# Kernel optimization log

Measured on AMD Instinct MI355X. Metric: run time of the kernel, lower is better.

## Reference

```python
import jax, jax.numpy as jnp
import numpy as np


def sym_logm(x):
    # matrix log of symmetric positive-definite matrices via eigh
    w, v = jnp.linalg.eigh(x)
    return jnp.einsum('...ik,...k,...jk->...ij', v, jnp.log(w), v)


def olm_diffeo(x):
    s = sym_logm(x)
    L = jnp.tril(s, -1)
    return L + L.swapaxes(-1, -2)


def cayley_map(X):
    I = jnp.eye(X.shape[-1], dtype=X.dtype)
    return (I - X) @ jnp.linalg.inv(I + X)


def trans_base(W, y):
    # C = cayley(skew(W)); y -> sym off-diagonal part of C y C^T
    C = cayley_map(W - W.T)
    y = jnp.einsum('pq,bnqr,sr->bnps', C, y, C)
    L = jnp.tril(y, -1)
    return L + L.swapaxes(-1, -2)


def setup_inputs() -> dict:
    B, N, n = 16, 512, 32
    key = jax.random.key(0)
    k1, k2, k3, k4 = jax.random.split(key, 4)
    A = jax.random.normal(k1, (B, N, n, n), dtype=jnp.float32)
    cov = A @ A.swapaxes(-1, -2) / n + jnp.eye(n, dtype=jnp.float32)
    d = jnp.sqrt(jnp.diagonal(cov, axis1=-2, axis2=-1))
    x = cov / (d[..., :, None] * d[..., None, :])  # SPD correlation matrices
    q_weight = jax.random.normal(k2, (n, n), dtype=jnp.float32) * 2.0 - 1.0
    k_weight = jax.random.normal(k3, (n, n), dtype=jnp.float32) * 2.0 - 1.0
    v_weight = jax.random.normal(k4, (n, n), dtype=jnp.float32) * 2.0 - 1.0
    return {"x": x, "q_weight": q_weight, "k_weight": k_weight, "v_weight": v_weight}


def reference(x, q_weight, k_weight, v_weight):
    xl = olm_diffeo(x)                       # [B,N,n,n]
    q = trans_base(q_weight, xl)
    k = trans_base(k_weight, xl)
    v = trans_base(v_weight, xl)
    B, N, n, _ = q.shape
    qf = q.reshape(B, N, n * n)
    kf = k.reshape(B, N, n * n)
    # energy[b,j,i] = ||q_i - k_j||_F  (Gram trick instead of [B,N,N,n,n] broadcast)
    q2 = jnp.sum(qf * qf, axis=-1)
    k2 = jnp.sum(kf * kf, axis=-1)
    d2 = q2[:, None, :] + k2[:, :, None] - 2.0 * jnp.einsum('bjf,bif->bji', kf, qf)
    energy = jnp.sqrt(jnp.maximum(d2, 1e-12))
    scores = 1.0 / (1.0 + jnp.log1p(energy))
    p = jax.nn.softmax(scores, axis=-2)      # softmax over j (dim -2), as in torch
    attn = p.swapaxes(-1, -2)                # [b, i, j]
    # out[b,c] = sum_a v[b,a] * attn[b,a,c]  (faithful to torch broadcast+sum(dim=1))
    return jnp.einsum('bac,baij->bcij', attn, v)
```

## Files before the change

### kernel.cpp

```cpp
#include <hip/hip_runtime.h>
#include <math.h>

#define NB 16
#define NSQ 512
#define NMAT (NB*NSQ)
#define NF 1024
#define NSWEEP 7
#define SB 36

__global__ __launch_bounds__(64) void cayley_kernel(
    const float* __restrict__ qw, const float* __restrict__ kw,
    const float* __restrict__ vw, float* __restrict__ Cout) {
  __shared__ float M[32][33];
  __shared__ float R[32][33];
  __shared__ float fac[32];
  const float* W = (blockIdx.x == 0) ? qw : ((blockIdx.x == 1) ? kw : vw);
  const int t = threadIdx.x;
  for (int idx = t; idx < 1024; idx += 64) {
    int i = idx >> 5, j = idx & 31;
    float xv = W[i*32+j] - W[j*32+i];
    float d = (i == j) ? 1.0f : 0.0f;
    M[i][j] = d - xv;
    R[i][j] = d + xv;
  }
  __syncthreads();
  for (int k = 0; k < 32; ++k) {
    float inv = 1.0f / M[k][k];
    __syncthreads();
    if (t < 32) M[k][t] *= inv; else R[k][t-32] *= inv;
    __syncthreads();
    if (t < 32) fac[t] = M[t][k];
    __syncthreads();
    if (t < 32) {
      float mk = M[k][t];
      for (int i = 0; i < 32; ++i) {
        if (i == k) continue;
        M[i][t] -= fac[i] * mk;
      }
    } else {
      int tc = t - 32;
      float rk = R[k][tc];
      for (int i = 0; i < 32; ++i) {
        if (i == k) continue;
        R[i][tc] -= fac[i] * rk;
      }
    }
    __syncthreads();
  }
  for (int idx = t; idx < 1024; idx += 64) {
    int p = idx >> 5, q = idx & 31;
    Cout[blockIdx.x * 1024 + idx] = R[q][p];
  }
}

__global__ __launch_bounds__(64) void logm_qkv_kernel(
    const float* __restrict__ x, const float* __restrict__ Cm,
    float* __restrict__ qo, float* __restrict__ ko, float* __restrict__ vo,
    float* __restrict__ q2, float* __restrict__ k2) {
  __shared__ __align__(16) float buf0[32*SB];
  __shared__ __align__(16) float buf1[32*SB];
  __shared__ __align__(16) float buf2[32*SB];
  __shared__ __align__(16) float2 cs[16];
  __shared__ __align__(16) float lw[32];
  const int t = threadIdx.x;
  const int m = blockIdx.x;
  const float* xm = x + (size_t)m * NF;

  #pragma unroll
  for (int s = 0; s < 4; ++s) {
    int fi = t + 64*s;
    int i = fi >> 3, j4 = (fi & 7) << 2;
    float4 xv = *(const float4*)&xm[(size_t)fi*4];
    *(float4*)&buf0[i*SB + j4] = xv;
    float4 iv;
    iv.x = (i == j4+0) ? 1.0f : 0.0f;
    iv.y = (i == j4+1) ? 1.0f : 0.0f;
    iv.z = (i == j4+2) ? 1.0f : 0.0f;
    iv.w = (i == j4+3) ? 1.0f : 0.0f;
    *(float4*)&buf1[i*SB + j4] = iv;
  }
  __syncthreads();

  const int ab = t >> 4;
  const int bI = t & 15;
  const int pi = ab & 1;

  for (int sw = 0; sw < NSWEEP; ++sw) {
    for (int r = 1; r < 32; ++r) {
      const int h = 31 - __builtin_clz((unsigned)r);
      const int lowmask = (1 << h) - 1;
      if (t < 16) {
        int p = ((t >> h) << (h+1)) | (t & lowmask);
        int q = p ^ r;
        float apq = buf0[p*SB+q];
        float c = 1.0f, s = 0.0f;
        if (fabsf(apq) > 1e-36f) {
          float app = buf0[p*SB+p];
          float aqq = buf0[q*SB+q];
          float tau = (aqq - app) / (2.0f * apq);
          float tt = 1.0f / (fabsf(tau) + sqrtf(1.0f + tau*tau));
          tt = (tau < 0.0f) ? -tt : tt;
          c = 1.0f / sqrtf(1.0f + tt*tt);
          s = tt * c;
        }
        cs[t] = make_float2(c, s);
      }
      __syncthreads();
      if (r == 1) {
        #pragma unroll
        for (int vtk = 0; vtk < 2; ++vtk) {
          int tsk = t + 64*vtk;
          int pr = tsk >> 3;
          int ch = (tsk & 7) << 2;
          int p = pr << 1;
          int q = p | 1;
          float2 c2 = cs[pr];
          float4 ap = *(float4*)&buf0[p*SB + ch];
          float4 aq = *(float4*)&buf0[q*SB + ch];
          float4 np, nq;
          np.x = c2.x*ap.x - c2.y*aq.x;  nq.x = fmaf(c2.y, ap.x, c2.x*aq.x);
          np.y = c2.x*ap.y - c2.y*aq.y;  nq.y = fmaf(c2.y, ap.y, c2.x*aq.y);
          np.z = c2.x*ap.z - c2.y*aq.z;  nq.z = fmaf(c2.y, ap.z, c2.x*aq.z);
          np.w = c2.x*ap.w - c2.y*aq.w;  nq.w = fmaf(c2.y, ap.w, c2.x*aq.w);
          *(float4*)&buf0[p*SB + ch] = np;
          *(float4*)&buf0[q*SB + ch] = nq;
        }
        __syncthreads();
        #pragma unroll
        for (int s4 = 0; s4 < 4; ++s4) {
          int tsk = t + 64*s4;
          int i = tsk >> 3;
          int cch = tsk & 7;
          float2 cA = cs[2*cch];
          float2 cB = cs[2*cch+1];
          float4 y = *(float4*)&buf0[i*SB + 4*cch];
          float4 z;
          z.x = cA.x*y.x - cA.y*y.y;  z.y = fmaf(cA.y, y.x, cA.x*y.y);
          z.z = cB.x*y.z - cB.y*y.w;  z.w = fmaf(cB.y, y.z, cB.x*y.w);
          *(float4*)&buf0[i*SB + 4*cch] = z;
        }
      } else {
        int pb = ((bI >> h) << (h+1)) | (bI & lowmask);
        int qb = pb ^ r;
        if (pi) { int tmp = pb; pb = qb; qb = tmp; }
        const float2 cb2 = cs[bI];
        const float cbb = cb2.x;
        const float sbb = pi ? -cb2.y : cb2.y;
        #pragma unroll
        for (int u = 0; u < 4; ++u) {
          int a = ab + 4*u;
          int pa = ((a >> h) << (h+1)) | (a & lowmask);
          int qa = pa ^ r;
          if (pi) { int tmp = pa; pa = qa; qa = tmp; }
          float2 ca2 = cs[a];
          float caa = ca2.x;
          float saa = pi ? -ca2.y : ca2.y;
          float* rp = buf0 + pa*SB;
          float* rq = buf0 + qa*SB;
          float x11 = rp[pb], x12 = rp[qb];
          float x21 = rq[pb], x22 = rq[qb];
          float y11 = caa*x11 - saa*x21;
          float y12 = caa*x12 - saa*x22;
          float y21 = fmaf(saa, x11, caa*x21);
          float y22 = fmaf(saa, x12, caa*x22);
          rp[pb] = cbb*y11 - sbb*y12;
          rp[qb] = fmaf(sbb, y11, cbb*y12);
          rq[pb] = cbb*y21 - sbb*y22;
          rq[qb] = fmaf(sbb, y21, cbb*y22);
        }
      }
      #pragma unroll
      for (int vtk = 0; vtk < 2; ++vtk) {
        int tsk = t + 64*vtk;
        int pr = tsk >> 3;
        int ch = (tsk & 7) << 2;
        int p = ((pr >> h) << (h+1)) | (pr & lowmask);
        int q = p ^ r;
        float2 c2 = cs[pr];
        float4 vp = *(float4*)&buf1[p*SB + ch];
        float4 vq = *(float4*)&buf1[q*SB + ch];
        float4 np, nq;
        np.x = c2.x*vp.x - c2.y*vq.x;  nq.x = fmaf(c2.y, vp.x, c2.x*vq.x);
        np.y = c2.x*vp.y - c2.y*vq.y;  nq.y = fmaf(c2.y, vp.y, c2.x*vq.y);
        np.z = c2.x*vp.z - c2.y*vq.z;  nq.z = fmaf(c2.y, vp.z, c2.x*vq.z);
        np.w = c2.x*vp.w - c2.y*vq.w;  nq.w = fmaf(c2.y, vp.w, c2.x*vq.w);
        *(float4*)&buf1[p*SB + ch] = np;
        *(float4*)&buf1[q*SB + ch] = nq;
      }
      __syncthreads();
    }
  }

  if (t < 32) lw[t] = logf(fmaxf(buf0[t*SB+t], 1e-30f));
  __syncthreads();
  #pragma unroll
  for (int s = 0; s < 16; ++s) {
    int idx = t + 64*s;
    int i = idx >> 5, k = idx & 31;
    buf0[i*SB + k] = buf1[k*SB + i];
  }
  __syncthreads();

  const int rg = t >> 3, cg = t & 7;
  const int i0 = rg*4, j0 = cg*4;
  {
    float acc[4][4] = {};
    #pragma unroll
    for (int k4 = 0; k4 < 32; k4 += 4) {
      float4 lv = *(float4*)&lw[k4];
      float4 av[4], bv[4];
      #pragma unroll
      for (int d = 0; d < 4; ++d) {
        float4 a4 = *(float4*)&buf0[(i0+d)*SB + k4];
        av[d].x = a4.x*lv.x; av[d].y = a4.y*lv.y; av[d].z = a4.z*lv.z; av[d].w = a4.w*lv.w;
        bv[d] = *(float4*)&buf0[(j0+d)*SB + k4];
      }
      #pragma unroll
      for (int d = 0; d < 4; ++d)
        #pragma unroll
        for (int e = 0; e < 4; ++e) {
          acc[d][e] = fmaf(av[d].x, bv[e].x, acc[d][e]);
          acc[d][e] = fmaf(av[d].y, bv[e].y, acc[d][e]);
          acc[d][e] = fmaf(av[d].z, bv[e].z, acc[d][e]);
          acc[d][e] = fmaf(av[d].w, bv[e].w, acc[d][e]);
        }
    }
    #pragma unroll
    for (int d = 0; d < 4; ++d) {
      if (rg == cg) acc[d][d] = 0.0f;
      float4 z; z.x = acc[d][0]; z.y = acc[d][1]; z.z = acc[d][2]; z.w = acc[d][3];
      *(float4*)&buf1[(i0+d)*SB + j0] = z;
    }
  }
  __syncthreads();

  for (int w = 0; w < 3; ++w) {
    const float* Cw = Cm + w*1024;
    #pragma unroll
    for (int s = 0; s < 4; ++s) {
      int fi = t + 64*s;
      int i = fi >> 3, c4 = (fi & 7) << 2;
      *(float4*)&buf0[i*SB + c4] = *(const float4*)&Cw[fi*4];
    }
    __syncthreads();
    {
      float acc[4][4] = {};
      #pragma unroll
      for (int k4 = 0; k4 < 32; k4 += 4) {
        float4 av[4], bv[4];
        #pragma unroll
        for (int d = 0; d < 4; ++d) {
          av[d] = *(float4*)&buf0[(i0+d)*SB + k4];
          bv[d] = *(float4*)&buf1[(j0+d)*SB + k4];
        }
        #pragma unroll
        for (int d = 0; d < 4; ++d)
          #pragma unroll
          for (int e = 0; e < 4; ++e) {
            acc[d][e] = fmaf(av[d].x, bv[e].x, acc[d][e]);
            acc[d][e] = fmaf(av[d].y, bv[e].y, acc[d][e]);
            acc[d][e] = fmaf(av[d].z, bv[e].z, acc[d][e]);
            acc[d][e] = fmaf(av[d].w, bv[e].w, acc[d][e]);
          }
      }
      #pragma unroll
      for (int d = 0; d < 4; ++d) {
        float4 z; z.x = acc[d][0]; z.y = acc[d][1]; z.z = acc[d][2]; z.w = acc[d][3];
        *(float4*)&buf2[(i0+d)*SB + j0] = z;
      }
    }
    __syncthreads();
    {
      float acc[4][4] = {};
      #pragma unroll
      for (int k4 = 0; k4 < 32; k4 += 4) {
        float4 av[4], bv[4];
        #pragma unroll
        for (int d = 0; d < 4; ++d) {
          av[d] = *(float4*)&buf2[(i0+d)*SB + k4];
          bv[d] = *(float4*)&buf0[(j0+d)*SB + k4];
        }
        #pragma unroll
        for (int d = 0; d < 4; ++d)
          #pragma unroll
          for (int e = 0; e < 4; ++e) {
            acc[d][e] = fmaf(av[d].x, bv[e].x, acc[d][e]);
            acc[d][e] = fmaf(av[d].y, bv[e].y, acc[d][e]);
            acc[d][e] = fmaf(av[d].z, bv[e].z, acc[d][e]);
            acc[d][e] = fmaf(av[d].w, bv[e].w, acc[d][e]);
          }
      }
      float ss = 0.0f;
      float* outp = (w == 0) ? qo : ((w == 1) ? ko : vo);
      #pragma unroll
      for (int d = 0; d < 4; ++d) {
        if (rg == cg) acc[d][d] = 0.0f;
        ss = fmaf(acc[d][0], acc[d][0], ss);
        ss = fmaf(acc[d][1], acc[d][1], ss);
        ss = fmaf(acc[d][2], acc[d][2], ss);
        ss = fmaf(acc[d][3], acc[d][3], ss);
        float4 z; z.x = acc[d][0]; z.y = acc[d][1]; z.z = acc[d][2]; z.w = acc[d][3];
        *(float4*)&outp[(size_t)m*NF + (i0+d)*32 + j0] = z;
      }
      if (w < 2) {
        #pragma unroll
        for (int off = 32; off > 0; off >>= 1)
          ss += __shfl_down(ss, off);
        if (t == 0) ((w == 0) ? q2 : k2)[m] = ss;
      }
    }
    __syncthreads();
  }
}

__global__ __launch_bounds__(256) void scores_kernel(
    const float* __restrict__ qf, const float* __restrict__ kf,
    const float* __restrict__ q2, const float* __restrict__ k2,
    float* __restrict__ P) {
  __shared__ float Ks[64][17];
  __shared__ float Qs[64][17];
  const int b = blockIdx.z;
  const int j0 = blockIdx.y * 64;
  const int i0 = blockIdx.x * 64;
  const int tx = threadIdx.x & 15, ty = threadIdx.x >> 4;
  const int lrow = threadIdx.x >> 2;
  const int lc4 = (threadIdx.x & 3) * 4;
  float acc[4][4] = {};
  const float* kb = kf + (size_t)(b*NSQ + j0) * NF;
  const float* qb = qf + (size_t)(b*NSQ + i0) * NF;
  for (int f0 = 0; f0 < NF; f0 += 16) {
    float4 kv = *(const float4*)(kb + (size_t)lrow*NF + f0 + lc4);
    float4 qv = *(const float4*)(qb + (size_t)lrow*NF + f0 + lc4);
    Ks[lrow][lc4+0] = kv.x; Ks[lrow][lc4+1] = kv.y; Ks[lrow][lc4+2] = kv.z; Ks[lrow][lc4+3] = kv.w;
    Qs[lrow][lc4+0] = qv.x; Qs[lrow][lc4+1] = qv.y; Qs[lrow][lc4+2] = qv.z; Qs[lrow][lc4+3] = qv.w;
    __syncthreads();
    #pragma unroll
    for (int kk = 0; kk < 16; ++kk) {
      float a0 = Ks[ty*4+0][kk], a1 = Ks[ty*4+1][kk], a2 = Ks[ty*4+2][kk], a3 = Ks[ty*4+3][kk];
      float b0 = Qs[tx*4+0][kk], b1 = Qs[tx*4+1][kk], b2 = Qs[tx*4+2][kk], b3 = Qs[tx*4+3][kk];
      acc[0][0]=fmaf(a0,b0,acc[0][0]); acc[0][1]=fmaf(a0,b1,acc[0][1]);
      acc[0][2]=fmaf(a0,b2,acc[0][2]); acc[0][3]=fmaf(a0,b3,acc[0][3]);
      acc[1][0]=fmaf(a1,b0,acc[1][0]); acc[1][1]=fmaf(a1,b1,acc[1][1]);
      acc[1][2]=fmaf(a1,b2,acc[1][2]); acc[1][3]=fmaf(a1,b3,acc[1][3]);
      acc[2][0]=fmaf(a2,b0,acc[2][0]); acc[2][1]=fmaf(a2,b1,acc[2][1]);
      acc[2][2]=fmaf(a2,b2,acc[2][2]); acc[2][3]=fmaf(a2,b3,acc[2][3]);
      acc[3][0]=fmaf(a3,b0,acc[3][0]); acc[3][1]=fmaf(a3,b1,acc[3][1]);
      acc[3][2]=fmaf(a3,b2,acc[3][2]); acc[3][3]=fmaf(a3,b3,acc[3][3]);
    }
    __syncthreads();
  }
  #pragma unroll
  for (int u = 0; u < 4; ++u) {
    int j = j0 + ty*4 + u;
    float kj = k2[b*NSQ + j];
    #pragma unroll
    for (int vv = 0; vv < 4; ++vv) {
      int i = i0 + tx*4 + vv;
      float d2 = kj + q2[b*NSQ + i] - 2.0f * acc[u][vv];
      float e = sqrtf(fmaxf(d2, 1e-12f));
      float sc = 1.0f / (1.0f + log1pf(e));
      P[(size_t)(b*NSQ + j)*NSQ + i] = sc;
    }
  }
}

__global__ __launch_bounds__(256) void softmax_kernel(float* __restrict__ P) {
  __shared__ float red[4][64];
  const int b = blockIdx.x >> 3;
  const int i0 = (blockIdx.x & 7) * 64;
  const int il = threadIdx.x & 63;
  const int jg = threadIdx.x >> 6;
  float* base = P + (size_t)b*NSQ*NSQ + i0 + il;
  float mx = -1e30f;
  for (int j = jg*128; j < jg*128 + 128; ++j)
    mx = fmaxf(mx, base[(size_t)j*NSQ]);
  red[jg][il] = mx;
  __syncthreads();
  float cm = fmaxf(fmaxf(red[0][il], red[1][il]), fmaxf(red[2][il], red[3][il]));
  float ssum = 0.0f;
  for (int j = jg*128; j < jg*128 + 128; ++j)
    ssum += expf(base[(size_t)j*NSQ] - cm);
  __syncthreads();
  red[jg][il] = ssum;
  __syncthreads();
  float inv = 1.0f / (red[0][il] + red[1][il] + red[2][il] + red[3][il]);
  for (int j = jg*128; j < jg*128 + 128; ++j) {
    size_t o = (size_t)j*NSQ;
    base[o] = expf(base[o] - cm) * inv;
  }
}

__global__ __launch_bounds__(256) void out_gemm_kernel(
    const float* __restrict__ P, const float* __restrict__ vf,
    float* __restrict__ out) {
  __shared__ float Ps[64][17];
  __shared__ float Vs[16][68];
  const int b = blockIdx.z;
  const int c0 = blockIdx.y * 64;
  const int f0 = blockIdx.x * 64;
  const int tx = threadIdx.x & 15, ty = threadIdx.x >> 4;
  float acc[4][4] = {};
  const float* Pb = P + (size_t)b * NSQ * NSQ;
  const float* Vb = vf + (size_t)b * NSQ * NF;
  for (int a0 = 0; a0 < NSQ; a0 += 16) {
    {
      int row = threadIdx.x >> 2;
      int c4 = (threadIdx.x & 3) * 4;
      float4 pv = *(const float4*)(Pb + (size_t)(c0 + row) * NSQ + a0 + c4);
      Ps[row][c4+0]=pv.x; Ps[row][c4+1]=pv.y; Ps[row][c4+2]=pv.z; Ps[row][c4+3]=pv.w;
    }
    {
      int row = threadIdx.x >> 4;
      int c4 = (threadIdx.x & 15) * 4;
      float4 vv4 = *(const float4*)(Vb + (size_t)(a0 + row) * NF + f0 + c4);
      Vs[row][c4+0]=vv4.x; Vs[row][c4+1]=vv4.y; Vs[row][c4+2]=vv4.z; Vs[row][c4+3]=vv4.w;
    }
    __syncthreads();
    #pragma unroll
    for (int kk = 0; kk < 16; ++kk) {
      float a0r = Ps[ty*4+0][kk], a1r = Ps[ty*4+1][kk], a2r = Ps[ty*4+2][kk], a3r = Ps[ty*4+3][kk];
      float b0 = Vs[kk][tx*4+0], b1 = Vs[kk][tx*4+1], b2 = Vs[kk][tx*4+2], b3 = Vs[kk][tx*4+3];
      acc[0][0]=fmaf(a0r,b0,acc[0][0]); acc[0][1]=fmaf(a0r,b1,acc[0][1]);
      acc[0][2]=fmaf(a0r,b2,acc[0][2]); acc[0][3]=fmaf(a0r,b3,acc[0][3]);
      acc[1][0]=fmaf(a1r,b0,acc[1][0]); acc[1][1]=fmaf(a1r,b1,acc[1][1]);
      acc[1][2]=fmaf(a1r,b2,acc[1][2]); acc[1][3]=fmaf(a1r,b3,acc[1][3]);
      acc[2][0]=fmaf(a2r,b0,acc[2][0]); acc[2][1]=fmaf(a2r,b1,acc[2][1]);
      acc[2][2]=fmaf(a2r,b2,acc[2][2]); acc[2][3]=fmaf(a2r,b3,acc[2][3]);
      acc[3][0]=fmaf(a3r,b0,acc[3][0]); acc[3][1]=fmaf(a3r,b1,acc[3][1]);
      acc[3][2]=fmaf(a3r,b2,acc[3][2]); acc[3][3]=fmaf(a3r,b3,acc[3][3]);
    }
    __syncthreads();
  }
  #pragma unroll
  for (int u = 0; u < 4; ++u) {
    float4 o;
    o.x = acc[u][0]; o.y = acc[u][1]; o.z = acc[u][2]; o.w = acc[u][3];
    *(float4*)(out + (size_t)(b*NSQ + c0 + ty*4 + u) * NF + f0 + tx*4) = o;
  }
}

extern "C" void kernel_launch(void* const* d_in, const int* in_sizes, int n_in,
                              void* d_out, int out_size, void* d_ws, size_t ws_size,
                              hipStream_t stream) {
  const float* x  = (const float*)d_in[0];
  const float* qw = (const float*)d_in[1];
  const float* kw = (const float*)d_in[2];
  const float* vw = (const float*)d_in[3];
  float* ws = (float*)d_ws;
  float* C  = ws;
  float* q  = ws + 3072;
  float* k  = q + (size_t)NMAT * NF;
  float* v  = k + (size_t)NMAT * NF;
  float* q2 = v + (size_t)NMAT * NF;
  float* k2 = q2 + NMAT;
  float* P  = k2 + NMAT;
  float* out = (float*)d_out;

  cayley_kernel<<<dim3(3), dim3(64), 0, stream>>>(qw, kw, vw, C);
  logm_qkv_kernel<<<dim3(NMAT), dim3(64), 0, stream>>>(x, C, q, k, v, q2, k2);
  scores_kernel<<<dim3(8, 8, NB), dim3(256), 0, stream>>>(q, k, q2, k2, P);
  softmax_kernel<<<dim3(NB * 8), dim3(256), 0, stream>>>(P);
  out_gemm_kernel<<<dim3(16, 8, NB), dim3(256), 0, stream>>>(P, v, out);
}
```

Before: 1.533 ms.

## Fold log-eigen reconstruction into per-weight transform using diagonal correction

Rather than forming the symmetric log matrix S = V diag(log w) V^T, zeroing its diagonal, and then computing C S C^T, the kernel computes D = C V directly and evaluates D diag(log w) D^T minus a correction term C diag(sd) C^T, where sd is the diagonal of S. This removes the explicit transpose and the separate 32x32x32 reconstruction GEMM and frees one shared buffer. Launch bounds now request 4 blocks per CU. In exchange, each of the three weight passes does an extra correction matmul. Subtracting large terms may also change rounding slightly.

New measurement: 2.517 ms. 1.64x slower.

```diff
diff --git a/kernel.cpp b/kernel.cpp
--- a/kernel.cpp
+++ b/kernel.cpp
@@ -53,15 +53,15 @@
   }
 }
 
-__global__ __launch_bounds__(64) void logm_qkv_kernel(
+__global__ __launch_bounds__(64, 4) void logm_qkv_kernel(
     const float* __restrict__ x, const float* __restrict__ Cm,
     float* __restrict__ qo, float* __restrict__ ko, float* __restrict__ vo,
     float* __restrict__ q2, float* __restrict__ k2) {
   __shared__ __align__(16) float buf0[32*SB];
   __shared__ __align__(16) float buf1[32*SB];
-  __shared__ __align__(16) float buf2[32*SB];
   __shared__ __align__(16) float2 cs[16];
   __shared__ __align__(16) float lw[32];
+  __shared__ __align__(16) float sd[32];
   const int t = threadIdx.x;
   const int m = blockIdx.x;
   const float* xm = x + (size_t)m * NF;
@@ -193,47 +193,18 @@
 
   if (t < 32) lw[t] = logf(fmaxf(buf0[t*SB+t], 1e-30f));
   __syncthreads();
-  #pragma unroll
-  for (int s = 0; s < 16; ++s) {
-    int idx = t + 64*s;
-    int i = idx >> 5, k = idx & 31;
-    buf0[i*SB + k] = buf1[k*SB + i];
+  if (t < 32) {
+    float s = 0.0f;
+    for (int k = 0; k < 32; ++k) {
+      float vv = buf1[k*SB + t];
+      s = fmaf(vv*vv, lw[k], s);
+    }
+    sd[t] = s;
   }
   __syncthreads();
 
   const int rg = t >> 3, cg = t & 7;
   const int i0 = rg*4, j0 = cg*4;
-  {
-    float acc[4][4] = {};
-    #pragma unroll
-    for (int k4 = 0; k4 < 32; k4 += 4) {
-      float4 lv = *(float4*)&lw[k4];
-      float4 av[4], bv[4];
-      #pragma unroll
-      for (int d = 0; d < 4; ++d) {
-        float4 a4 = *(float4*)&buf0[(i0+d)*SB + k4];
-        av[d].x = a4.x*lv.x; av[d].y = a4.y*lv.y; av[d].z = a4.z*lv.z; av[d].w = a4.w*lv.w;
-        bv[d] = *(float4*)&buf0[(j0+d)*SB + k4];
-      }
-      #pragma unroll
-      for (int d = 0; d < 4; ++d)
-        #pragma unroll
-        for (int e = 0; e < 4; ++e) {
-          acc[d][e] = fmaf(av[d].x, bv[e].x, acc[d][e]);
-          acc[d][e] = fmaf(av[d].y, bv[e].y, acc[d][e]);
-          acc[d][e] = fmaf(av[d].z, bv[e].z, acc[d][e]);
-          acc[d][e] = fmaf(av[d].w, bv[e].w, acc[d][e]);
-        }
-    }
-    #pragma unroll
-    for (int d = 0; d < 4; ++d) {
-      if (rg == cg) acc[d][d] = 0.0f;
-      float4 z; z.x = acc[d][0]; z.y = acc[d][1]; z.z = acc[d][2]; z.w = acc[d][3];
-      *(float4*)&buf1[(i0+d)*SB + j0] = z;
-    }
-  }
-  __syncthreads();
-
   for (int w = 0; w < 3; ++w) {
     const float* Cw = Cm + w*1024;
     #pragma unroll
@@ -243,57 +214,62 @@
       *(float4*)&buf0[i*SB + c4] = *(const float4*)&Cw[fi*4];
     }
     __syncthreads();
+    float dacc[4][4] = {};
+    float corr[4][4] = {};
+    #pragma unroll
+    for (int l4 = 0; l4 < 32; l4 += 4) {
+      float4 sv = *(float4*)&sd[l4];
+      float4 av[4], bv[4], cv[4];
+      #pragma unroll
+      for (int d = 0; d < 4; ++d) {
+        av[d] = *(float4*)&buf1[(i0+d)*SB + l4];
+        bv[d] = *(float4*)&buf0[(j0+d)*SB + l4];
+        float4 c4v = *(float4*)&buf0[(i0+d)*SB + l4];
+        cv[d].x = c4v.x*sv.x; cv[d].y = c4v.y*sv.y; cv[d].z = c4v.z*sv.z; cv[d].w = c4v.w*sv.w;
+      }
+      #pragma unroll
+      for (int d = 0; d < 4; ++d)
+        #pragma unroll
+        for (int e = 0; e < 4; ++e) {
+          dacc[d][e] = fmaf(av[d].x, bv[e].x, dacc[d][e]);
+          dacc[d][e] = fmaf(av[d].y, bv[e].y, dacc[d][e]);
+          dacc[d][e] = fmaf(av[d].z, bv[e].z, dacc[d][e]);
+          dacc[d][e] = fmaf(av[d].w, bv[e].w, dacc[d][e]);
+          corr[d][e] = fmaf(cv[d].x, bv[e].x, corr[d][e]);
+          corr[d][e] = fmaf(cv[d].y, bv[e].y, corr[d][e]);
+          corr[d][e] = fmaf(cv[d].z, bv[e].z, corr[d][e]);
+          corr[d][e] = fmaf(cv[d].w, bv[e].w, corr[d][e]);
+        }
+    }
+    __syncthreads();
+    #pragma unroll
+    for (int d = 0; d < 4; ++d) {
+      float4 z; z.x = dacc[d][0]; z.y = dacc[d][1]; z.z = dacc[d][2]; z.w = dacc[d][3];
+      *(float4*)&buf0[(i0+d)*SB + j0] = z;
+    }
+    __syncthreads();
     {
       float acc[4][4] = {};
-      #pragma unroll
-      for (int k4 = 0; k4 < 32; k4 += 4) {
-        float4 av[4], bv[4];
-        #pragma unroll
-        for (int d = 0; d < 4; ++d) {
-          av[d] = *(float4*)&buf0[(i0+d)*SB + k4];
-          bv[d] = *(float4*)&buf1[(j0+d)*SB + k4];
-        }
-        #pragma unroll
-        for (int d = 0; d < 4; ++d)
-          #pragma unroll
-          for (int e = 0; e < 4; ++e) {
-            acc[d][e] = fmaf(av[d].x, bv[e].x, acc[d][e]);
-            acc[d][e] = fmaf(av[d].y, bv[e].y, acc[d][e]);
-            acc[d][e] = fmaf(av[d].z, bv[e].z, acc[d][e]);
-            acc[d][e] = fmaf(av[d].w, bv[e].w, acc[d][e]);
-          }
-      }
-      #pragma unroll
-      for (int d = 0; d < 4; ++d) {
-        float4 z; z.x = acc[d][0]; z.y = acc[d][1]; z.z = acc[d][2]; z.w = acc[d][3];
-        *(float4*)&buf2[(i0+d)*SB + j0] = z;
-      }
-    }
-    __syncthreads();
-    {
-      float acc[4][4] = {};
-      #pragma unroll
-      for (int k4 = 0; k4 < 32; k4 += 4) {
-        float4 av[4], bv[4];
-        #pragma unroll
-        for (int d = 0; d < 4; ++d) {
-          av[d] = *(float4*)&buf2[(i0+d)*SB + k4];
-          bv[d] = *(float4*)&buf0[(j0+d)*SB + k4];
-        }
-        #pragma unroll
-        for (int d = 0; d < 4; ++d)
-          #pragma unroll
-          for (int e = 0; e < 4; ++e) {
-            acc[d][e] = fmaf(av[d].x, bv[e].x, acc[d][e]);
-            acc[d][e] = fmaf(av[d].y, bv[e].y, acc[d][e]);
-            acc[d][e] = fmaf(av[d].z, bv[e].z, acc[d][e]);
-            acc[d][e] = fmaf(av[d].w, bv[e].w, acc[d][e]);
-          }
+      for (int k = 0; k < 32; ++k) {
+        float lwk = lw[k];
+        float4 a4 = *(float4*)&buf0[k*SB + i0];
+        float4 b4 = *(float4*)&buf0[k*SB + j0];
+        float4 as; as.x = a4.x*lwk; as.y = a4.y*lwk; as.z = a4.z*lwk; as.w = a4.w*lwk;
+        acc[0][0]=fmaf(as.x,b4.x,acc[0][0]); acc[0][1]=fmaf(as.x,b4.y,acc[0][1]);
+        acc[0][2]=fmaf(as.x,b4.z,acc[0][2]); acc[0][3]=fmaf(as.x,b4.w,acc[0][3]);
+        acc[1][0]=fmaf(as.y,b4.x,acc[1][0]); acc[1][1]=fmaf(as.y,b4.y,acc[1][1]);
+        acc[1][2]=fmaf(as.y,b4.z,acc[1][2]); acc[1][3]=fmaf(as.y,b4.w,acc[1][3]);
+        acc[2][0]=fmaf(as.z,b4.x,acc[2][0]); acc[2][1]=fmaf(as.z,b4.y,acc[2][1]);
+        acc[2][2]=fmaf(as.z,b4.z,acc[2][2]); acc[2][3]=fmaf(as.z,b4.w,acc[2][3]);
+        acc[3][0]=fmaf(as.w,b4.x,acc[3][0]); acc[3][1]=fmaf(as.w,b4.y,acc[3][1]);
+        acc[3][2]=fmaf(as.w,b4.z,acc[3][2]); acc[3][3]=fmaf(as.w,b4.w,acc[3][3]);
       }
       float ss = 0.0f;
       float* outp = (w == 0) ? qo : ((w == 1) ? ko : vo);
       #pragma unroll
       for (int d = 0; d < 4; ++d) {
+        #pragma unroll
+        for (int e = 0; e < 4; ++e) acc[d][e] -= corr[d][e];
         if (rg == cg) acc[d][d] = 0.0f;
         ss = fmaf(acc[d][0], acc[d][0], ss);
         ss = fmaf(acc[d][1], acc[d][1], ss);
```
